# Kernel tuning notes

Hardware: AMD Instinct MI355X
Metric: run time of the kernel (lower is better)

## Reference

```python
import jax, jax.numpy as jnp
import numpy as np

B, GX, GY = 4, 480, 360
C_IN, C_OUT = 64, 32
N = 480000

def setup_inputs() -> dict:
    key = jax.random.key(0)
    k1, k2, k3, k4, k5 = jax.random.split(key, 5)
    pt_fea = jax.random.normal(k1, (N, C_IN), dtype=jnp.float32)
    pt_ind = jax.random.randint(k2, (N, 2), 0, 360, dtype=jnp.int32)
    batch_idx = jax.random.randint(k3, (N,), 0, B, dtype=jnp.int32)
    W_comp = jax.random.normal(k4, (C_IN, C_OUT), dtype=jnp.float32) * 0.1
    b_comp = jax.random.normal(k5, (C_OUT,), dtype=jnp.float32) * 0.1
    return {"pt_fea": pt_fea, "pt_ind": pt_ind, "batch_idx": batch_idx,
            "W_comp": W_comp, "b_comp": b_comp}

def reference(pt_fea, pt_ind, batch_idx, W_comp, b_comp):
    # Linearized voxel key: (batch, x, y) -> flat segment id.
    # torch.unique + scatter_max over unique voxels followed by fancy-index
    # scatter into a zero grid is equivalent to a dense segment_max with
    # empty voxels forced to zero.
    seg = (batch_idx.astype(jnp.int32) * (GX * GY)
           + pt_ind[:, 0] * GY + pt_ind[:, 1])  # [N]
    num_seg = B * GX * GY
    pooled = jax.ops.segment_max(pt_fea, seg, num_segments=num_seg)  # [BV, C_IN]
    cnt = jax.ops.segment_sum(jnp.ones((pt_fea.shape[0],), jnp.float32), seg,
                              num_segments=num_seg)  # [BV]
    occupied = (cnt > 0)[:, None]
    pooled = jnp.where(occupied, pooled, 0.0)  # neutralize -inf of empty voxels
    # fea_compression: Linear + ReLU, applied to occupied voxels only
    comp = jax.nn.relu(pooled @ W_comp + b_comp)  # [BV, C_OUT]
    comp = jnp.where(occupied, comp, 0.0)
    out = comp.reshape(B, GX, GY, C_OUT)
    return jnp.transpose(out, (0, 3, 1, 2))  # [B, C_OUT, GX, GY]
```

## Files before the change

### kernel.cpp

```cpp
#include <hip/hip_runtime.h>

#define GXGY  172800
#define NSEG  691200
#define CIN   64
#define COUT  32
#define VPB   64
#define PSTR  65

__global__ __launch_bounds__(256) void build_lists_kernel(
    const int* __restrict__ ind,
    const int* __restrict__ bidx,
    int*       __restrict__ head,
    int*       __restrict__ next,
    int N)
{
    int i = blockIdx.x * 256 + threadIdx.x;
    if (i >= N) return;
    int2 xy = ((const int2*)ind)[i];
    int seg = bidx[i] * GXGY + xy.x * 360 + xy.y;
    next[i] = atomicExch(&head[seg], i);
}

__global__ __launch_bounds__(256) void pool_compress_kernel(
    const float* __restrict__ fea,
    const int*   __restrict__ head,
    const int*   __restrict__ next,
    const float* __restrict__ W,
    const float* __restrict__ bias,
    float*       __restrict__ out)
{
    __shared__ float sP[VPB * PSTR];
    __shared__ int   sOcc[VPB];

    int tid  = threadIdx.x;
    int wid  = tid >> 6;
    int lane = tid & 63;
    int sub  = lane >> 4;
    int sl   = lane & 15;

    int vbase = blockIdx.x * VPB;

    int heads = (lane < 16) ? head[vbase + wid * 16 + lane] : -1;

    int idx[4];
    #pragma unroll
    for (int q = 0; q < 4; ++q) idx[q] = __shfl(heads, q * 4 + sub);

    unsigned occm = 0;
    #pragma unroll
    for (int q = 0; q < 4; ++q) if (idx[q] >= 0) occm |= (1u << q);

    if (sl == 0) {
        #pragma unroll
        for (int q = 0; q < 4; ++q)
            sOcc[wid * 16 + q * 4 + sub] = (occm >> q) & 1u;
    }

    float4 m[4];
    #pragma unroll
    for (int q = 0; q < 4; ++q) {
        if (idx[q] >= 0) {
            m[q] = *((const float4*)(fea + (size_t)idx[q] * CIN) + sl);
            idx[q] = next[idx[q]];
        }
    }
    while (idx[0] >= 0 || idx[1] >= 0 || idx[2] >= 0 || idx[3] >= 0) {
        #pragma unroll
        for (int q = 0; q < 4; ++q) {
            if (idx[q] >= 0) {
                float4 t = *((const float4*)(fea + (size_t)idx[q] * CIN) + sl);
                m[q].x = fmaxf(m[q].x, t.x);
                m[q].y = fmaxf(m[q].y, t.y);
                m[q].z = fmaxf(m[q].z, t.z);
                m[q].w = fmaxf(m[q].w, t.w);
                idx[q] = next[idx[q]];
            }
        }
    }
    #pragma unroll
    for (int q = 0; q < 4; ++q) {
        if (occm & (1u << q)) {
            int lv = wid * 16 + q * 4 + sub;
            float* dst = &sP[lv * PSTR + sl * 4];
            dst[0] = m[q].x; dst[1] = m[q].y; dst[2] = m[q].z; dst[3] = m[q].w;
        }
    }
    __syncthreads();

    int lv = lane;
    int g  = __builtin_amdgcn_readfirstlane(wid);
    int b  = vbase / GXGY;
    int rem = vbase - b * GXGY + lv;

    const float* Wg = W + g * 8;
    const float* bg = bias + g * 8;

    float res[8];
    if (sOcc[lv]) {
        float acc[8];
        #pragma unroll
        for (int c = 0; c < 8; ++c) acc[c] = bg[c];
        #pragma unroll 16
        for (int k = 0; k < CIN; ++k) {
            float p = sP[lv * PSTR + k];
            #pragma unroll
            for (int c = 0; c < 8; ++c)
                acc[c] = fmaf(p, Wg[k * COUT + c], acc[c]);
        }
        #pragma unroll
        for (int c = 0; c < 8; ++c) res[c] = fmaxf(acc[c], 0.0f);
    } else {
        #pragma unroll
        for (int c = 0; c < 8; ++c) res[c] = 0.0f;
    }

    float* op = out + (size_t)b * COUT * GXGY + (size_t)g * 8 * GXGY + rem;
    #pragma unroll
    for (int c = 0; c < 8; ++c) op[c * GXGY] = res[c];
}

extern "C" void kernel_launch(void* const* d_in, const int* in_sizes, int n_in,
                              void* d_out, int out_size, void* d_ws, size_t ws_size,
                              hipStream_t stream)
{
    const float* fea  = (const float*)d_in[0];
    const int*   ind  = (const int*)d_in[1];
    const int*   bidx = (const int*)d_in[2];
    const float* W    = (const float*)d_in[3];
    const float* bias = (const float*)d_in[4];
    float*       out  = (float*)d_out;

    int N = in_sizes[0] / CIN;

    int* head = (int*)d_ws;
    int* next = (int*)d_ws + NSEG;

    hipMemsetAsync(head, 0xFF, (size_t)NSEG * sizeof(int), stream);
    build_lists_kernel<<<(N + 255) / 256, 256, 0, stream>>>(ind, bidx, head, next, N);
    pool_compress_kernel<<<NSEG / VPB, 256, 0, stream>>>(fea, head, next, W, bias, out);
}
```

Before: 255.1 us.

## Replace linked-list voxel grouping with counting-sort CSR layout

Swaps the atomicExch linked-list build for a count / two-level prefix scan / fill pipeline that produces a CSR array of point indices per voxel. The pool kernel then reads contiguous index ranges, staged per wave in shared memory, instead of chasing dependent next[] pointers, which removes the serial latency chain in the gather loop. In exchange it adds three kernel launches and a second atomic pass over all points.

```diff
diff --git a/kernel.cpp b/kernel.cpp
--- a/kernel.cpp
+++ b/kernel.cpp
@@ -6,31 +6,96 @@
 #define COUT  32
 #define VPB   64
 #define PSTR  65
-
-__global__ __launch_bounds__(256) void build_lists_kernel(
+#define NTILE 675
+
+
+__global__ __launch_bounds__(256) void count_kernel(
     const int* __restrict__ ind,
     const int* __restrict__ bidx,
-    int*       __restrict__ head,
-    int*       __restrict__ next,
+    int*       __restrict__ cnt,
     int N)
 {
     int i = blockIdx.x * 256 + threadIdx.x;
     if (i >= N) return;
     int2 xy = ((const int2*)ind)[i];
     int seg = bidx[i] * GXGY + xy.x * 360 + xy.y;
-    next[i] = atomicExch(&head[seg], i);
+    atomicAdd(&cnt[seg], 1);
+}
+
+__global__ __launch_bounds__(256) void scan_tile_kernel(
+    int* __restrict__ cnt, int* __restrict__ tsum)
+{
+    int t = threadIdx.x;
+    int base = blockIdx.x * 256 + t;
+    int4 c = ((const int4*)cnt)[base];
+    int s = c.x + c.y + c.z + c.w;
+
+    int lane = t & 63, wid = t >> 6;
+    int v = s;
+    #pragma unroll
+    for (int d = 1; d < 64; d <<= 1) {
+        int u = __shfl_up(v, d);
+        if (lane >= d) v += u;
+    }
+    __shared__ int wsum[4];
+    if (lane == 63) wsum[wid] = v;
+    __syncthreads();
+    int wbase = 0;
+    #pragma unroll
+    for (int w = 0; w < 3; ++w) if (w < wid) wbase += wsum[w];
+
+    int excl = wbase + v - s;
+    int4 o; o.x = excl; o.y = o.x + c.x; o.z = o.y + c.y; o.w = o.z + c.z;
+    ((int4*)cnt)[base] = o;
+    if (t == 255) tsum[blockIdx.x] = excl + s;
+}
+
+__global__ __launch_bounds__(256) void scan_totals_kernel(int* __restrict__ tsum)
+{
+    __shared__ int buf[1024];
+    int t = threadIdx.x;
+    for (int j = t; j < 1024; j += 256) buf[j] = (j < NTILE) ? tsum[j] : 0;
+    __syncthreads();
+    for (int d = 1; d < 1024; d <<= 1) {
+        int vals[4];
+        #pragma unroll
+        for (int k = 0; k < 4; ++k) { int j = t + k * 256; vals[k] = (j >= d) ? buf[j - d] : 0; }
+        __syncthreads();
+        #pragma unroll
+        for (int k = 0; k < 4; ++k) { int j = t + k * 256; buf[j] += vals[k]; }
+        __syncthreads();
+    }
+    for (int j = t; j < NTILE; j += 256) tsum[j] = (j == 0) ? 0 : buf[j - 1];
+}
+
+__global__ __launch_bounds__(256) void fill_kernel(
+    const int* __restrict__ ind,
+    const int* __restrict__ bidx,
+    int*       __restrict__ cnt,
+    const int* __restrict__ tsum,
+    int*       __restrict__ csr,
+    int N)
+{
+    int i = blockIdx.x * 256 + threadIdx.x;
+    if (i >= N) return;
+    int2 xy = ((const int2*)ind)[i];
+    int seg = bidx[i] * GXGY + xy.x * 360 + xy.y;
+    int pos = atomicAdd(&cnt[seg], 1) + tsum[seg >> 10];
+    csr[pos] = i;
 }
 
 __global__ __launch_bounds__(256) void pool_compress_kernel(
     const float* __restrict__ fea,
-    const int*   __restrict__ head,
-    const int*   __restrict__ next,
+    const int*   __restrict__ cnt,
+    const int*   __restrict__ tsum,
+    const int*   __restrict__ csr,
     const float* __restrict__ W,
     const float* __restrict__ bias,
     float*       __restrict__ out)
 {
     __shared__ float sP[VPB * PSTR];
-    __shared__ int   sOcc[VPB];
+    __shared__ int   sLen[VPB];
+    __shared__ int   sIdx[4][64];
 
     int tid  = threadIdx.x;
     int wid  = tid >> 6;
@@ -39,51 +104,54 @@
     int sl   = lane & 15;
 
     int vbase = blockIdx.x * VPB;
-
-    int heads = (lane < 16) ? head[vbase + wid * 16 + lane] : -1;
-
-    int idx[4];
-    #pragma unroll
-    for (int q = 0; q < 4; ++q) idx[q] = __shfl(heads, q * 4 + sub);
-
-    unsigned occm = 0;
-    #pragma unroll
-    for (int q = 0; q < 4; ++q) if (idx[q] >= 0) occm |= (1u << q);
-
-    if (sl == 0) {
-        #pragma unroll
-        for (int q = 0; q < 4; ++q)
-            sOcc[wid * 16 + q * 4 + sub] = (occm >> q) & 1u;
-    }
+    int v0    = vbase + wid * 16;
+
+    int o = 0;
+    if (lane < 17) {
+        int vv = v0 - 1 + lane;
+        o = (vv < 0) ? 0 : (cnt[vv] + tsum[vv >> 10]);
+    }
+    int onext = __shfl(o, (lane + 1) & 63);
+    if (lane < 16) sLen[wid * 16 + lane] = onext - o;
+
+    int ws0 = __shfl(o, 0);
+    int wsE = __shfl(o, 16);
+    int cw  = wsE - ws0;
+    if (lane < min(cw, 64)) sIdx[wid][lane] = csr[ws0 + lane];
+
+    int stt[4], len[4];
+    #pragma unroll
+    for (int q = 0; q < 4; ++q) {
+        int a = __shfl(o, q * 4 + sub);
+        int b = __shfl(o, q * 4 + sub + 1);
+        stt[q] = a; len[q] = b - a;
+    }
+    int maxlen = max(max(len[0], len[1]), max(len[2], len[3]));
 
     float4 m[4];
     #pragma unroll
-    for (int q = 0; q < 4; ++q) {
-        if (idx[q] >= 0) {
-            m[q] = *((const float4*)(fea + (size_t)idx[q] * CIN) + sl);
-            idx[q] = next[idx[q]];
+    for (int q = 0; q < 4; ++q) if (len[q] > 0) {
+        int off = stt[q] - ws0;
+        int id  = (off < 64) ? sIdx[wid][off] : csr[stt[q]];
+        m[q] = ((const float4*)(fea + (size_t)id * CIN))[sl];
+    }
+    for (int r = 1; r < maxlen; ++r) {
+        #pragma unroll
+        for (int q = 0; q < 4; ++q) if (r < len[q]) {
+            int off = stt[q] - ws0 + r;
+            int id  = (off < 64) ? sIdx[wid][off] : csr[stt[q] + r];
+            float4 t = ((const float4*)(fea + (size_t)id * CIN))[sl];
+            m[q].x = fmaxf(m[q].x, t.x);
+            m[q].y = fmaxf(m[q].y, t.y);
+            m[q].z = fmaxf(m[q].z, t.z);
+            m[q].w = fmaxf(m[q].w, t.w);
         }
     }
-    while (idx[0] >= 0 || idx[1] >= 0 || idx[2] >= 0 || idx[3] >= 0) {
-        #pragma unroll
-        for (int q = 0; q < 4; ++q) {
-            if (idx[q] >= 0) {
-                float4 t = *((const float4*)(fea + (size_t)idx[q] * CIN) + sl);
-                m[q].x = fmaxf(m[q].x, t.x);
-                m[q].y = fmaxf(m[q].y, t.y);
-                m[q].z = fmaxf(m[q].z, t.z);
-                m[q].w = fmaxf(m[q].w, t.w);
-                idx[q] = next[idx[q]];
-            }
-        }
-    }
-    #pragma unroll
-    for (int q = 0; q < 4; ++q) {
-        if (occm & (1u << q)) {
-            int lv = wid * 16 + q * 4 + sub;
-            float* dst = &sP[lv * PSTR + sl * 4];
-            dst[0] = m[q].x; dst[1] = m[q].y; dst[2] = m[q].z; dst[3] = m[q].w;
-        }
+    #pragma unroll
+    for (int q = 0; q < 4; ++q) if (len[q] > 0) {
+        int lv = wid * 16 + q * 4 + sub;
+        float* dst = &sP[lv * PSTR + sl * 4];
+        dst[0] = m[q].x; dst[1] = m[q].y; dst[2] = m[q].z; dst[3] = m[q].w;
     }
     __syncthreads();
 
@@ -96,7 +164,7 @@
     const float* bg = bias + g * 8;
 
     float res[8];
-    if (sOcc[lv]) {
+    if (sLen[lv] > 0) {
         float acc[8];
         #pragma unroll
         for (int c = 0; c < 8; ++c) acc[c] = bg[c];
@@ -132,10 +200,14 @@
 
     int N = in_sizes[0] / CIN;
 
-    int* head = (int*)d_ws;
-    int* next = (int*)d_ws + NSEG;
-
-    hipMemsetAsync(head, 0xFF, (size_t)NSEG * sizeof(int), stream);
-    build_lists_kernel<<<(N + 255) / 256, 256, 0, stream>>>(ind, bidx, head, next, N);
-    pool_compress_kernel<<<NSEG / VPB, 256, 0, stream>>>(fea, head, next, W, bias, out);
-}
+    int* cnt  = (int*)d_ws;
+    int* tsum = cnt + NSEG;
+    int* csr  = tsum + 1024;
+
+    hipMemsetAsync(cnt, 0, (size_t)NSEG * sizeof(int), stream);
+    count_kernel<<<(N + 255) / 256, 256, 0, stream>>>(ind, bidx, cnt, N);
+    scan_tile_kernel<<<NTILE, 256, 0, stream>>>(cnt, tsum);
+    scan_totals_kernel<<<1, 256, 0, stream>>>(tsum);
+    fill_kernel<<<(N + 255) / 256, 256, 0, stream>>>(ind, bidx, cnt, tsum, csr, N);
+    pool_compress_kernel<<<NSEG / VPB, 256, 0, stream>>>(fea, cnt, tsum, csr, W, bias, out);
+}
```

New measurement: 294.8 us. 15.5% more time.

## Replace per-voxel linked lists with per-block bucketed binning and LDS atomic max

Applied to the files above, without the earlier changes.

Points are binned into fixed-capacity buckets per 64-voxel block (with a global spill list for overflow) instead of per-voxel linked lists. The pool kernel then loads the bucket's point ids into shared memory and reduces features with order-preserving unsigned atomicMax in LDS. This replaces serial pointer chasing through next[] with independent parallel gathers, and shrinks the memset from the full head array to the block counters. The cost is LDS atomic contention, an extra key-decode pass, and a spill scan that every block repeats whenever any bucket overflows.

```diff
diff --git a/kernel.cpp b/kernel.cpp
--- a/kernel.cpp
+++ b/kernel.cpp
@@ -2,91 +2,132 @@
 
 #define GXGY  172800
 #define NSEG  691200
+#define NBLK  10800
 #define CIN   64
 #define COUT  32
 #define VPB   64
 #define PSTR  65
+#define CAP   96
+#define SPILLCAP 8192
 
-__global__ __launch_bounds__(256) void build_lists_kernel(
+
+__device__ __forceinline__ unsigned fkey(float f) {
+    unsigned u = __float_as_uint(f);
+    return (u & 0x80000000u) ? ~u : (u | 0x80000000u);
+}
+__device__ __forceinline__ float funkey(unsigned k) {
+    unsigned u = (k & 0x80000000u) ? (k ^ 0x80000000u) : ~k;
+    return __uint_as_float(u);
+}
+
+__global__ __launch_bounds__(256) void bin_kernel(
     const int* __restrict__ ind,
     const int* __restrict__ bidx,
-    int*       __restrict__ head,
-    int*       __restrict__ next,
+    int*       __restrict__ bCnt,
+    int*       __restrict__ spillCnt,
+    int*       __restrict__ bucket,
+    int2*      __restrict__ spill,
     int N)
 {
     int i = blockIdx.x * 256 + threadIdx.x;
     if (i >= N) return;
     int2 xy = ((const int2*)ind)[i];
     int seg = bidx[i] * GXGY + xy.x * 360 + xy.y;
-    next[i] = atomicExch(&head[seg], i);
+    int blk = seg >> 6;
+    int enc = (i << 6) | (seg & 63);
+    int pos = atomicAdd(&bCnt[blk], 1);
+    if (pos < CAP) {
+        bucket[blk * CAP + pos] = enc;
+    } else {
+        int sp = atomicAdd(spillCnt, 1);
+        if (sp < SPILLCAP) spill[sp] = make_int2(blk, enc);
+    }
 }
 
 __global__ __launch_bounds__(256) void pool_compress_kernel(
     const float* __restrict__ fea,
-    const int*   __restrict__ head,
-    const int*   __restrict__ next,
+    const int*   __restrict__ bCnt,
+    const int*   __restrict__ spillCnt,
+    const int*   __restrict__ bucket,
+    const int2*  __restrict__ spill,
     const float* __restrict__ W,
     const float* __restrict__ bias,
     float*       __restrict__ out)
 {
-    __shared__ float sP[VPB * PSTR];
-    __shared__ int   sOcc[VPB];
+    __shared__ unsigned sK[VPB * PSTR];
+    __shared__ int      sOcc[VPB];
+    __shared__ int      sIds[CAP];
 
-    int tid  = threadIdx.x;
-    int wid  = tid >> 6;
-    int lane = tid & 63;
-    int sub  = lane >> 4;
-    int sl   = lane & 15;
+    int tid = threadIdx.x;
+    int blk = blockIdx.x;
+    int vbase = blk * VPB;
 
-    int vbase = blockIdx.x * VPB;
+    #pragma unroll
+    for (int j = 0; j < 17; ++j) {
+        int idx = tid + j * 256;
+        if (idx < VPB * PSTR) sK[idx] = 0u;
+    }
+    if (tid < VPB) sOcc[tid] = 0;
 
-    int heads = (lane < 16) ? head[vbase + wid * 16 + lane] : -1;
+    int nb = min(bCnt[blk], CAP);
+    if (tid < nb) sIds[tid] = bucket[blk * CAP + tid];
+    __syncthreads();
 
-    int idx[4];
-    #pragma unroll
-    for (int q = 0; q < 4; ++q) idx[q] = __shfl(heads, q * 4 + sub);
+    int sg = tid >> 4;
+    int sl = tid & 15;
+    for (int r0 = sg; r0 < nb; r0 += 64) {
+        int r1 = min(r0 + 16, nb - 1);
+        int r2 = min(r0 + 32, nb - 1);
+        int r3 = min(r0 + 48, nb - 1);
+        int e0 = sIds[r0], e1 = sIds[r1], e2 = sIds[r2], e3 = sIds[r3];
+        int l0 = e0 & 63, l1 = e1 & 63, l2 = e2 & 63, l3 = e3 & 63;
+        float4 t0 = ((const float4*)(fea + (size_t)(e0 >> 6) * CIN))[sl];
+        float4 t1 = ((const float4*)(fea + (size_t)(e1 >> 6) * CIN))[sl];
+        float4 t2 = ((const float4*)(fea + (size_t)(e2 >> 6) * CIN))[sl];
+        float4 t3 = ((const float4*)(fea + (size_t)(e3 >> 6) * CIN))[sl];
 
-    unsigned occm = 0;
-    #pragma unroll
-    for (int q = 0; q < 4; ++q) if (idx[q] >= 0) occm |= (1u << q);
-
-    if (sl == 0) {
-        #pragma unroll
-        for (int q = 0; q < 4; ++q)
-            sOcc[wid * 16 + q * 4 + sub] = (occm >> q) & 1u;
+        unsigned* p0 = &sK[l0 * PSTR + sl * 4];
+        atomicMax(p0 + 0, fkey(t0.x)); atomicMax(p0 + 1, fkey(t0.y));
+        atomicMax(p0 + 2, fkey(t0.z)); atomicMax(p0 + 3, fkey(t0.w));
+        unsigned* p1 = &sK[l1 * PSTR + sl * 4];
+        atomicMax(p1 + 0, fkey(t1.x)); atomicMax(p1 + 1, fkey(t1.y));
+        atomicMax(p1 + 2, fkey(t1.z)); atomicMax(p1 + 3, fkey(t1.w));
+        unsigned* p2 = &sK[l2 * PSTR + sl * 4];
+        atomicMax(p2 + 0, fkey(t2.x)); atomicMax(p2 + 1, fkey(t2.y));
+        atomicMax(p2 + 2, fkey(t2.z)); atomicMax(p2 + 3, fkey(t2.w));
+        unsigned* p3 = &sK[l3 * PSTR + sl * 4];
+        atomicMax(p3 + 0, fkey(t3.x)); atomicMax(p3 + 1, fkey(t3.y));
+        atomicMax(p3 + 2, fkey(t3.z)); atomicMax(p3 + 3, fkey(t3.w));
+        if (sl == 0) { sOcc[l0] = 1; sOcc[l1] = 1; sOcc[l2] = 1; sOcc[l3] = 1; }
     }
 
-    float4 m[4];
-    #pragma unroll
-    for (int q = 0; q < 4; ++q) {
-        if (idx[q] >= 0) {
-            m[q] = *((const float4*)(fea + (size_t)idx[q] * CIN) + sl);
-            idx[q] = next[idx[q]];
-        }
-    }
-    while (idx[0] >= 0 || idx[1] >= 0 || idx[2] >= 0 || idx[3] >= 0) {
-        #pragma unroll
-        for (int q = 0; q < 4; ++q) {
-            if (idx[q] >= 0) {
-                float4 t = *((const float4*)(fea + (size_t)idx[q] * CIN) + sl);
-                m[q].x = fmaxf(m[q].x, t.x);
-                m[q].y = fmaxf(m[q].y, t.y);
-                m[q].z = fmaxf(m[q].z, t.z);
-                m[q].w = fmaxf(m[q].w, t.w);
-                idx[q] = next[idx[q]];
+    int nsp = spillCnt[0];
+    if (nsp > 0) {
+        int ns = min(nsp, SPILLCAP);
+        for (int j = 0; j < ns; ++j) {
+            int2 e = spill[j];
+            if (e.x == blk && tid < 16) {
+                int lv = e.y & 63;
+                float4 t = ((const float4*)(fea + (size_t)(e.y >> 6) * CIN))[tid];
+                unsigned* p = &sK[lv * PSTR + tid * 4];
+                atomicMax(p + 0, fkey(t.x)); atomicMax(p + 1, fkey(t.y));
+                atomicMax(p + 2, fkey(t.z)); atomicMax(p + 3, fkey(t.w));
+                if (tid == 0) sOcc[lv] = 1;
             }
-        }
-    }
-    #pragma unroll
-    for (int q = 0; q < 4; ++q) {
-        if (occm & (1u << q)) {
-            int lv = wid * 16 + q * 4 + sub;
-            float* dst = &sP[lv * PSTR + sl * 4];
-            dst[0] = m[q].x; dst[1] = m[q].y; dst[2] = m[q].z; dst[3] = m[q].w;
         }
     }
     __syncthreads();
 
+    float* sP = (float*)sK;
+    #pragma unroll
+    for (int j = 0; j < 17; ++j) {
+        int idx = tid + j * 256;
+        if (idx < VPB * PSTR) sP[idx] = funkey(sK[idx]);
+    }
+    __syncthreads();
+
+    int wid  = tid >> 6;
+    int lane = tid & 63;
     int lv = lane;
     int g  = __builtin_amdgcn_readfirstlane(wid);
     int b  = vbase / GXGY;
@@ -132,10 +173,14 @@
 
     int N = in_sizes[0] / CIN;
 
-    int* head = (int*)d_ws;
-    int* next = (int*)d_ws + NSEG;
+    int* bCnt     = (int*)d_ws;
+    int* spillCnt = bCnt + NBLK;
+    int* bucket   = bCnt + 10816;
+    int2* spill   = (int2*)(bucket + NBLK * CAP);
 
-    hipMemsetAsync(head, 0xFF, (size_t)NSEG * sizeof(int), stream);
-    build_lists_kernel<<<(N + 255) / 256, 256, 0, stream>>>(ind, bidx, head, next, N);
-    pool_compress_kernel<<<NSEG / VPB, 256, 0, stream>>>(fea, head, next, W, bias, out);
+    hipMemsetAsync(bCnt, 0, 10816 * sizeof(int), stream);
+    bin_kernel<<<(N + 255) / 256, 256, 0, stream>>>(ind, bidx, bCnt, spillCnt,
+                                                    bucket, spill, N);
+    pool_compress_kernel<<<NBLK, 256, 0, stream>>>(fea, bCnt, spillCnt, bucket,
+                                                   spill, W, bias, out);
 }
```

Result: slower. 269.3 us (+5.5%).
